# Performance work log

Measured on AMD Instinct MI355X. Metric: run time of the kernel, lower is better.

The kernel has to match this reference:

```python
import jax, jax.numpy as jnp
import numpy as np

EPS = 1e-5  # BatchNorm1d default eps


def xyz2sphere(xyz):
    # xyz: (..., 3) -> (rho, theta/pi, phi/(2pi)+0.5)
    rho = jnp.sqrt(jnp.sum(xyz * xyz, axis=-1, keepdims=True))
    safe_rho = jnp.where(rho == 0, 1.0, rho)
    theta = jnp.arccos(jnp.clip(xyz[..., 2:3] / safe_rho, -1.0, 1.0))
    theta = jnp.where(rho == 0, 0.0, theta) / jnp.pi
    phi = jnp.arctan2(xyz[..., 1:2], xyz[..., 0:1]) / (2.0 * jnp.pi) + 0.5
    return jnp.concatenate([rho, theta, phi], axis=-1)


def _conv_bn_relu(x, w, b, g, be):
    # x: (M, nsample, Cin); 1x1 Conv1d == per-point linear over channel dim
    y = jnp.einsum('mnc,oc->mno', x, w) + b
    mean = jnp.mean(y, axis=(0, 1))
    var = jnp.var(y, axis=(0, 1))  # biased var, matches torch BN training mode
    return jax.nn.relu(g * (y - mean) * jax.lax.rsqrt(var + EPS) + be)


def setup_inputs() -> dict:
    N, NS, CF = 32768, 32, 64
    key = jax.random.key(0)
    ks = jax.random.split(key, 8)
    center = jax.random.normal(ks[0], (N, 3), dtype=jnp.float32)
    normal = jax.random.normal(ks[1], (N, 3), dtype=jnp.float32)
    feature = jax.random.normal(ks[2], (N, CF), dtype=jnp.float32)
    group_idx = jax.random.randint(ks[3], (N, NS), 0, N)
    offset = jnp.full((1,), N, dtype=jnp.int32)
    s = 0.05
    return {
        'center': center, 'normal': normal, 'feature': feature,
        'offset': offset, 'group_idx': group_idx,
        'w0': jax.random.normal(ks[4], (64, 73), dtype=jnp.float32) * s,
        'b0': jnp.zeros((64,), jnp.float32), 'g0': jnp.ones((64,), jnp.float32), 'be0': jnp.zeros((64,), jnp.float32),
        'w1': jax.random.normal(ks[5], (64, 64), dtype=jnp.float32) * s,
        'b1': jnp.zeros((64,), jnp.float32), 'g1': jnp.ones((64,), jnp.float32), 'be1': jnp.zeros((64,), jnp.float32),
        'w2': jax.random.normal(ks[6], (128, 64), dtype=jnp.float32) * s,
        'b2': jnp.zeros((128,), jnp.float32), 'g2': jnp.ones((128,), jnp.float32), 'be2': jnp.zeros((128,), jnp.float32),
    }


def reference(center, normal, feature, offset, group_idx,
              w0, b0, g0, be0, w1, b1, g1, be1, w2, b2, g2, be2):
    # stride=1: new_center == center, M == N
    group_center = center[group_idx]            # (M, NS, 3)
    group_normal = normal[group_idx]            # (M, NS, 3)
    gcn = group_center - center[:, None, :]     # center-relative coords
    gcn = jnp.concatenate([gcn, xyz2sphere(gcn)], axis=-1)  # return_polar=True -> (M, NS, 6)
    x = jnp.concatenate([gcn, group_normal, feature[group_idx]], axis=-1)  # (M, NS, 73)
    x = _conv_bn_relu(x, w0, b0, g0, be0)
    x = _conv_bn_relu(x, w1, b1, g1, be1)
    x = _conv_bn_relu(x, w2, b2, g2, be2)
    new_feature = jnp.max(x, axis=1)            # max-pool over neighborhood -> (M, 128)
    return (center, normal, new_feature, offset)
```

## Files before the change

### kernel.cpp

```cpp
#include <hip/hip_runtime.h>
#include <hip/hip_bf16.h>
#include <math.h>


typedef __attribute__((ext_vector_type(8))) short short8;
typedef __attribute__((ext_vector_type(4))) float f32x4;

constexpr int NS = 32;
constexpr int GRIDS = 1280;
constexpr float BN_EPS = 1e-5f;
constexpr float INV_PI  = 0.31830988618379067f;
constexpr float INV_2PI = 0.15915494309189535f;

__device__ __forceinline__ short cvt_bf16(float f) {
    unsigned u = __float_as_uint(f);
    u = (u + 0x7FFFu + ((u >> 16) & 1u)) >> 16;
    return (short)u;
}

__global__ __launch_bounds__(256) void feat2bf(
    const float* __restrict__ feature, short* __restrict__ fb, int n8)
{
    int i = blockIdx.x * 256 + threadIdx.x;
    if (i >= n8) return;
    const float4* src = (const float4*)(feature + (size_t)i * 8);
    float4 a = src[0], b = src[1];
    short8 v;
    v[0]=cvt_bf16(a.x); v[1]=cvt_bf16(a.y); v[2]=cvt_bf16(a.z); v[3]=cvt_bf16(a.w);
    v[4]=cvt_bf16(b.x); v[5]=cvt_bf16(b.y); v[6]=cvt_bf16(b.z); v[7]=cvt_bf16(b.w);
    *(short8*)(fb + (size_t)i * 8) = v;
}

__global__ __launch_bounds__(256) void prep_cn(
    const float* __restrict__ center, const float* __restrict__ normal,
    float* __restrict__ cn, int N)
{
    int i = blockIdx.x * 256 + threadIdx.x;
    if (i >= N) return;
    float4 a, b;
    a.x = center[i*3+0]; a.y = center[i*3+1]; a.z = center[i*3+2];
    a.w = normal[i*3+0];
    b.x = normal[i*3+1]; b.y = normal[i*3+2]; b.z = 0.f; b.w = 0.f;
    *(float4*)(cn + (size_t)i * 8)     = a;
    *(float4*)(cn + (size_t)i * 8 + 4) = b;
}

__global__ __launch_bounds__(256) void prep_weights(
    const float* __restrict__ w0, const float* __restrict__ w1,
    const float* __restrict__ w2,
    short* __restrict__ wf0, short* __restrict__ wf1, short* __restrict__ wf2)
{
    int i = blockIdx.x * 256 + threadIdx.x;
    int l = i & 63;
    int f = i >> 6;
    float vals[8];
    short* dh;
    if (f < 12) {
        int kt = f >> 2, nt = f & 3;
        int n = nt * 16 + (l & 15);
        int k0 = kt * 32 + (l >> 4) * 8;
        for (int j = 0; j < 8; ++j) {
            int kn = k0 + j;
            float v;
            if (kn < 64)       v = w0[n * 73 + 9 + kn];
            else if (kn < 70)  v = w0[n * 73 + (kn - 64)];
            else if (kn == 70) v = w0[n * 73 + 6];
            else if (kn == 72) v = w0[n * 73 + 7];
            else if (kn == 73) v = w0[n * 73 + 8];
            else v = 0.f;
            vals[j] = v;
        }
        dh = wf0 + (size_t)f * 512 + l * 8;
    } else if (f < 20) {
        int ff = f - 12;
        int kt = ff >> 2, nt = ff & 3;
        int n = nt * 16 + (l & 15);
        int k0 = kt * 32 + (l >> 4) * 8;
        for (int j = 0; j < 8; ++j) vals[j] = w1[n * 64 + k0 + j];
        dh = wf1 + (size_t)ff * 512 + l * 8;
    } else if (f < 36) {
        int ff = f - 20;
        int kt = ff >> 3, nt = ff & 7;
        int n = nt * 16 + (l & 15);
        int k0 = kt * 32 + (l >> 4) * 8;
        for (int j = 0; j < 8; ++j) vals[j] = w2[n * 64 + k0 + j];
        dh = wf2 + (size_t)ff * 512 + l * 8;
    } else return;
    for (int j = 0; j < 8; ++j) dh[j] = cvt_bf16(vals[j]);
}

template <int STAGE>
__global__ __launch_bounds__(256, (STAGE == 2 ? 4 : 5)) void stage_kernel(
    const float* __restrict__ center, const float* __restrict__ normal,
    const float* __restrict__ feature, const short* __restrict__ fb,
    const float* __restrict__ cn, const int* __restrict__ gidx,
    const short* __restrict__ wf0, const short* __restrict__ wf1,
    const short* __restrict__ wf2,
    const float* __restrict__ b0, const float* __restrict__ b1,
    const float* __restrict__ b2,
    const float* __restrict__ g0, const float* __restrict__ be0,
    const float* __restrict__ g1, const float* __restrict__ be1,
    const float* __restrict__ fstats, float* __restrict__ part,
    float* __restrict__ ymax, float* __restrict__ ymin,
    int ntiles, float inv_cnt)
{
    __shared__ __align__(16) short Xs[64 * 128];
    __shared__ __align__(16) short X1s[(STAGE >= 1) ? 64 * 64 : 16];

    const int t    = threadIdx.x;
    const int lane = t & 63;
    const int wv   = __builtin_amdgcn_readfirstlane(t >> 6);
    const int ln   = lane & 15;
    const int kg   = lane >> 4;
    const int rs   = ln & 7;
    const int chW  = wv * 16 + ln;

    short8 W0[3];
#pragma unroll
    for (int kt = 0; kt < 3; ++kt)
        W0[kt] = *(const short8*)(wf0 + (size_t)((kt*4 + wv) * 64 + lane) * 8);
    short8 W1[2];
    if constexpr (STAGE >= 1) {
#pragma unroll
        for (int kt = 0; kt < 2; ++kt)
            W1[kt] = *(const short8*)(wf1 + (size_t)((kt*4 + wv) * 64 + lane) * 8);
    }
    short8 W2[2][2];
    if constexpr (STAGE == 2) {
#pragma unroll
        for (int nti = 0; nti < 2; ++nti)
#pragma unroll
            for (int kt = 0; kt < 2; ++kt) {
                int ff = kt * 8 + (wv * 2 + nti);
                W2[nti][kt] = *(const short8*)(wf2 + (size_t)(ff * 64 + lane) * 8);
            }
    }

    const float bb0 = b0[chW];
    float bb1 = 0.f, bb2a = 0.f, bb2b = 0.f;
    float a0v = 0.f, c0v = 0.f, a1v = 0.f, c1v = 0.f;
    if constexpr (STAGE >= 1) {
        bb1 = b1[chW];
        float mean = fstats[chW] * inv_cnt;
        float var  = fstats[64 + chW] * inv_cnt - mean * mean;
        a0v = g0[chW] * rsqrtf(fmaxf(var, 0.f) + BN_EPS);
        c0v = be0[chW] - a0v * mean;
    }
    if constexpr (STAGE == 2) {
        bb2a = b2[wv * 32 + ln];
        bb2b = b2[wv * 32 + 16 + ln];
        float mean = fstats[128 + chW] * inv_cnt;
        float var  = fstats[192 + chW] * inv_cnt - mean * mean;
        a1v = g1[chW] * rsqrtf(fmaxf(var, 0.f) + BN_EPS);
        c1v = be1[chW] - a1v * mean;
    }

    if (t < 128) {
        int r = t >> 1, u = 10 + (t & 1);
        short8 z; z[0]=0;z[1]=0;z[2]=0;z[3]=0;z[4]=0;z[5]=0;z[6]=0;z[7]=0;
        *(short8*)(Xs + r * 128 + ((u ^ (r & 7)) * 8)) = z;
    }

    constexpr int NT = (STAGE == 2) ? 2 : 1;
    float ssum[NT], ssq[NT];
#pragma unroll
    for (int nt = 0; nt < NT; ++nt) { ssum[nt] = 0.f; ssq[nt] = 0.f; }

    for (int tile = blockIdx.x; tile < ntiles; tile += gridDim.x) {
        const int m0 = tile * 2;
        __syncthreads();
        {
            const int s = t & 63, h = wv;
            const int m = m0 + (s >> 5);
            const int j = gidx[m * NS + (s & 31)];
            short* xr = Xs + s * 128;
            const int rx = s & 7;
            if (fb) {
                const uint4* fp = (const uint4*)(fb + (size_t)j * 64);
                uint4 v0 = fp[2 * h], v1 = fp[2 * h + 1];
                *(uint4*)(xr + (((2 * h)     ^ rx) * 8)) = v0;
                *(uint4*)(xr + (((2 * h + 1) ^ rx) * 8)) = v1;
            } else {
                const float4* fp = (const float4*)(feature + (size_t)j * 64 + h * 16);
#pragma unroll
                for (int q = 0; q < 2; ++q) {
                    float4 a = fp[2 * q], b = fp[2 * q + 1];
                    short8 v;
                    v[0]=cvt_bf16(a.x); v[1]=cvt_bf16(a.y); v[2]=cvt_bf16(a.z); v[3]=cvt_bf16(a.w);
                    v[4]=cvt_bf16(b.x); v[5]=cvt_bf16(b.y); v[6]=cvt_bf16(b.z); v[7]=cvt_bf16(b.w);
                    *(short8*)(xr + (((2 * h + q) ^ rx) * 8)) = v;
                }
            }
            if (h == 0) {
                float cjx, cjy, cjz, nx, cmx, cmy, cmz;
                if (cn) {
                    float4 cj = *(const float4*)(cn + (size_t)j * 8);
                    float4 cm = *(const float4*)(cn + (size_t)m * 8);
                    cjx=cj.x; cjy=cj.y; cjz=cj.z; nx=cj.w;
                    cmx=cm.x; cmy=cm.y; cmz=cm.z;
                } else {
                    cjx=center[j*3+0]; cjy=center[j*3+1]; cjz=center[j*3+2];
                    nx=normal[j*3+0];
                    cmx=center[m*3+0]; cmy=center[m*3+1]; cmz=center[m*3+2];
                }
                float gx = cjx - cmx, gy = cjy - cmy, gz = cjz - cmz;
                float rho = sqrtf(gx*gx + gy*gy + gz*gz);
                float th = 0.f;
                if (rho > 0.f) th = acosf(fminf(1.f, fmaxf(-1.f, gz / rho))) * INV_PI;
                float ph = atan2f(gy, gx) * INV_2PI + 0.5f;
                short8 v;
                v[0]=cvt_bf16(gx);  v[1]=cvt_bf16(gy); v[2]=cvt_bf16(gz);
                v[3]=cvt_bf16(rho); v[4]=cvt_bf16(th); v[5]=cvt_bf16(ph);
                v[6]=cvt_bf16(nx);  v[7]=0;
                *(short8*)(xr + ((8 ^ rx) * 8)) = v;
            } else if (h == 1) {
                float ny, nz;
                if (cn) {
                    float4 w = *(const float4*)(cn + (size_t)j * 8 + 4);
                    ny = w.x; nz = w.y;
                } else {
                    ny = normal[j*3+1]; nz = normal[j*3+2];
                }
                short8 v; v[0]=cvt_bf16(ny); v[1]=cvt_bf16(nz);
                v[2]=0;v[3]=0;v[4]=0;v[5]=0;v[6]=0;v[7]=0;
                *(short8*)(xr + ((9 ^ rx) * 8)) = v;
            }
        }
        __syncthreads();
#pragma unroll 2
        for (int mt = 0; mt < 4; ++mt) {
            const short* arow = Xs + (mt * 16 + ln) * 128;
            f32x4 acc = {bb0, bb0, bb0, bb0};
#pragma unroll
            for (int kt = 0; kt < 3; ++kt) {
                short8 A = *(const short8*)(arow + (((kt*4 + kg) ^ rs) * 8));
                acc = __builtin_amdgcn_mfma_f32_16x16x32_bf16(A, W0[kt], acc, 0, 0, 0);
            }
            if constexpr (STAGE == 0) {
#pragma unroll
                for (int r = 0; r < 4; ++r) {
                    float y = acc[r];
                    ssum[0] += y; ssq[0] += y * y;
                }
            } else {
#pragma unroll
                for (int r = 0; r < 4; ++r) {
                    int row = mt * 16 + kg * 4 + r;
                    float x1 = fmaxf(a0v * acc[r] + c0v, 0.f);
                    X1s[row * 64 + ((((chW >> 3) ^ (row & 7)) << 3) | (chW & 7))] = cvt_bf16(x1);
                }
            }
        }
        if constexpr (STAGE >= 1) {
            __syncthreads();
#pragma unroll 2
            for (int mt = 0; mt < 4; ++mt) {
                const short* arow = X1s + (mt * 16 + ln) * 64;
                f32x4 acc = {bb1, bb1, bb1, bb1};
#pragma unroll
                for (int kt = 0; kt < 2; ++kt) {
                    short8 A = *(const short8*)(arow + (((kt*4 + kg) ^ rs) * 8));
                    acc = __builtin_amdgcn_mfma_f32_16x16x32_bf16(A, W1[kt], acc, 0, 0, 0);
                }
                if constexpr (STAGE == 1) {
#pragma unroll
                    for (int r = 0; r < 4; ++r) {
                        float y = acc[r];
                        ssum[0] += y; ssq[0] += y * y;
                    }
                } else {
#pragma unroll
                    for (int r = 0; r < 4; ++r) {
                        int row = mt * 16 + kg * 4 + r;
                        float x2 = fmaxf(a1v * acc[r] + c1v, 0.f);
                        Xs[row * 128 + ((((chW >> 3) ^ (row & 7)) << 3) | (chW & 7))] = cvt_bf16(x2);
                    }
                }
            }
        }
        if constexpr (STAGE == 2) {
            __syncthreads();
#pragma unroll
            for (int p = 0; p < 2; ++p) {
                float mx0 = -3.402823466e38f, mn0 = 3.402823466e38f;
                float mx1 = -3.402823466e38f, mn1 = 3.402823466e38f;
#pragma unroll
                for (int mh = 0; mh < 2; ++mh) {
                    const int mt = p * 2 + mh;
                    const short* arow = Xs + (mt * 16 + ln) * 128;
                    short8 A0 = *(const short8*)(arow + (((kg)     ^ rs) * 8));
                    short8 A1 = *(const short8*)(arow + (((4 + kg) ^ rs) * 8));
                    f32x4 acc = {bb2a, bb2a, bb2a, bb2a};
                    acc = __builtin_amdgcn_mfma_f32_16x16x32_bf16(A0, W2[0][0], acc, 0, 0, 0);
                    acc = __builtin_amdgcn_mfma_f32_16x16x32_bf16(A1, W2[0][1], acc, 0, 0, 0);
#pragma unroll
                    for (int r = 0; r < 4; ++r) {
                        float y = acc[r];
                        ssum[0] += y; ssq[0] += y * y;
                        mx0 = fmaxf(mx0, y); mn0 = fminf(mn0, y);
                    }
                    f32x4 acd = {bb2b, bb2b, bb2b, bb2b};
                    acd = __builtin_amdgcn_mfma_f32_16x16x32_bf16(A0, W2[1][0], acd, 0, 0, 0);
                    acd = __builtin_amdgcn_mfma_f32_16x16x32_bf16(A1, W2[1][1], acd, 0, 0, 0);
#pragma unroll
                    for (int r = 0; r < 4; ++r) {
                        float y = acd[r];
                        ssum[1] += y; ssq[1] += y * y;
                        mx1 = fmaxf(mx1, y); mn1 = fminf(mn1, y);
                    }
                }
                mx0 = fmaxf(mx0, __shfl_xor(mx0, 16)); mn0 = fminf(mn0, __shfl_xor(mn0, 16));
                mx0 = fmaxf(mx0, __shfl_xor(mx0, 32)); mn0 = fminf(mn0, __shfl_xor(mn0, 32));
                mx1 = fmaxf(mx1, __shfl_xor(mx1, 16)); mn1 = fminf(mn1, __shfl_xor(mn1, 16));
                mx1 = fmaxf(mx1, __shfl_xor(mx1, 32)); mn1 = fminf(mn1, __shfl_xor(mn1, 32));
                if (lane < 16) {
                    size_t base = (size_t)(m0 + p) * 128 + wv * 32 + ln;
                    ymax[base]      = mx0; ymin[base]      = mn0;
                    ymax[base + 16] = mx1; ymin[base + 16] = mn1;
                }
            }
        }
    }

    float* pb = part + (size_t)blockIdx.x * 256;
#pragma unroll
    for (int nt = 0; nt < NT; ++nt) {
        float v = ssum[nt], q = ssq[nt];
        v += __shfl_xor(v, 16); q += __shfl_xor(q, 16);
        v += __shfl_xor(v, 32); q += __shfl_xor(q, 32);
        if (lane < 16) {
            constexpr int NCH = (STAGE == 2) ? 128 : 64;
            int c = (STAGE == 2) ? (wv * 32 + nt * 16 + ln) : (wv * 16 + ln);
            pb[c] = v; pb[NCH + c] = q;
        }
    }
}

__global__ __launch_bounds__(256) void reduce_partials(
    const float* __restrict__ part, float* __restrict__ fstats,
    int base, int nblocks)
{
    __shared__ float red[256];
    int c = blockIdx.x;
    float s = 0.f;
    for (int b = threadIdx.x; b < nblocks; b += 256)
        s += part[(size_t)b * 256 + c];
    red[threadIdx.x] = s;
    __syncthreads();
    for (int off = 128; off > 0; off >>= 1) {
        if (threadIdx.x < off) red[threadIdx.x] += red[threadIdx.x + off];
        __syncthreads();
    }
    if (threadIdx.x == 0) fstats[base + c] = red[0];
}

__global__ __launch_bounds__(256) void final_kernel(
    const float* __restrict__ center, const float* __restrict__ normal,
    const int* __restrict__ offs,
    const float* __restrict__ g2, const float* __restrict__ be2,
    const float* __restrict__ fstats,
    const float* __restrict__ ymax, const float* __restrict__ ymin,
    float* __restrict__ out, int N, float inv_cnt)
{
    int i = blockIdx.x * 256 + threadIdx.x;
    int nc = N * 3;
    int nf = N * 128;
    int total = 2 * nc + nf + 1;
    if (i >= total) return;
    if (i < nc) {
        out[i] = center[i];
    } else if (i < 2 * nc) {
        out[i] = normal[i - nc];
    } else if (i < 2 * nc + nf) {
        int idx = i - 2 * nc;
        int c = idx & 127;
        float mean = fstats[256 + c] * inv_cnt;
        float var  = fstats[384 + c] * inv_cnt - mean * mean;
        float a = g2[c] * rsqrtf(fmaxf(var, 0.f) + BN_EPS);
        float v = (a >= 0.f) ? ymax[idx] : ymin[idx];
        out[i] = fmaxf(a * (v - mean) + be2[c], 0.f);
    } else {
        out[i] = (float)offs[0];
    }
}

extern "C" void kernel_launch(void* const* d_in, const int* in_sizes, int n_in,
                              void* d_out, int out_size, void* d_ws, size_t ws_size,
                              hipStream_t stream)
{
    const float* center  = (const float*)d_in[0];
    const float* normal  = (const float*)d_in[1];
    const float* feature = (const float*)d_in[2];
    const int*   offs    = (const int*)d_in[3];
    const int*   gidx    = (const int*)d_in[4];
    const float* w0  = (const float*)d_in[5];
    const float* b0  = (const float*)d_in[6];
    const float* g0  = (const float*)d_in[7];
    const float* be0 = (const float*)d_in[8];
    const float* w1  = (const float*)d_in[9];
    const float* b1  = (const float*)d_in[10];
    const float* g1  = (const float*)d_in[11];
    const float* be1 = (const float*)d_in[12];
    const float* w2  = (const float*)d_in[13];
    const float* b2  = (const float*)d_in[14];
    const float* g2  = (const float*)d_in[15];
    const float* be2 = (const float*)d_in[16];

    const int N = in_sizes[0] / 3;
    const int ntiles = N / 2;
    const float inv_cnt = 1.0f / (float)((size_t)N * NS);

    float* out = (float*)d_out;
    float* out_nf = out + (size_t)2 * N * 3;

    float* wsf    = (float*)d_ws;
    float* fstats = wsf;
    float* part   = wsf + 512;
    float* ymin   = part + (size_t)GRIDS * 256;
    short* wbase  = (short*)(ymin + (size_t)N * 128);
    short* wf0 = wbase;
    short* wf1 = wf0 + 12 * 512;
    short* wf2 = wf1 + 8 * 512;
    short* wend = wf2 + 16 * 512;

    short* featbf = wend;
    float* cn     = (float*)(featbf + (size_t)N * 64);
    size_t need = (size_t)((char*)(cn + (size_t)N * 8) - (char*)d_ws);
    const bool has_tab = (ws_size >= need);
    const short* fbp = has_tab ? featbf : nullptr;
    const float* cnp = has_tab ? cn : nullptr;

    dim3 blk(256);

    prep_weights<<<dim3(9), blk, 0, stream>>>(w0, w1, w2, wf0, wf1, wf2);
    if (has_tab) {
        int n8 = N * 8;
        feat2bf<<<dim3((n8 + 255) / 256), blk, 0, stream>>>(feature, featbf, n8);
        prep_cn<<<dim3((N + 255) / 256), blk, 0, stream>>>(center, normal, cn, N);
    }

    stage_kernel<0><<<dim3(GRIDS), blk, 0, stream>>>(center, normal, feature,
        fbp, cnp, gidx, wf0, wf1, wf2, b0, b1, b2,
        g0, be0, g1, be1, fstats, part, out_nf, ymin, ntiles, inv_cnt);
    reduce_partials<<<dim3(128), blk, 0, stream>>>(part, fstats, 0, GRIDS);

    stage_kernel<1><<<dim3(GRIDS), blk, 0, stream>>>(center, normal, feature,
        fbp, cnp, gidx, wf0, wf1, wf2, b0, b1, b2,
        g0, be0, g1, be1, fstats, part, out_nf, ymin, ntiles, inv_cnt);
    reduce_partials<<<dim3(128), blk, 0, stream>>>(part, fstats, 128, GRIDS);

    stage_kernel<2><<<dim3(GRIDS), blk, 0, stream>>>(center, normal, feature,
        fbp, cnp, gidx, wf0, wf1, wf2, b0, b1, b2,
        g0, be0, g1, be1, fstats, part, out_nf, ymin, ntiles, inv_cnt);
    reduce_partials<<<dim3(256), blk, 0, stream>>>(part, fstats, 256, GRIDS);

    int total = 2 * N * 3 + N * 128 + 1;
    final_kernel<<<dim3((total + 255) / 256), blk, 0, stream>>>(
        center, normal, offs, g2, be2, fstats, out_nf, ymin, out, N, inv_cnt);
}
```

Before: 225.4 us.

## Load gathered features straight into MFMA operand registers, skip LDS staging

Gathered bf16 feature rows are now read directly from global memory into the MFMA A-operand registers instead of first being written to a 64x128 shared tile. Only the small geometry/normal part (16 channels) still goes through a compact padded shared buffer, and stage 2 gets its own X2s buffer for layer-2 activations. The intent is to drop LDS write/read traffic and shrink shared memory for better occupancy. The trade-off is more scattered global loads issued per lane, which may hurt coalescing. Stage 2 also moves to a smaller grid.

```diff
diff --git a/kernel.cpp b/kernel.cpp
--- a/kernel.cpp
+++ b/kernel.cpp
@@ -7,7 +7,8 @@
 typedef __attribute__((ext_vector_type(4))) float f32x4;
 
 constexpr int NS = 32;
-constexpr int GRIDS = 1280;
+constexpr int GRID01 = 1280;
+constexpr int GRID2  = 1024;
 constexpr float BN_EPS = 1e-5f;
 constexpr float INV_PI  = 0.31830988618379067f;
 constexpr float INV_2PI = 0.15915494309189535f;
@@ -104,8 +105,9 @@
     float* __restrict__ ymax, float* __restrict__ ymin,
     int ntiles, float inv_cnt)
 {
-    __shared__ __align__(16) short Xs[64 * 128];
+    __shared__ __align__(16) short Xg[64 * 20 + 16];
     __shared__ __align__(16) short X1s[(STAGE >= 1) ? 64 * 64 : 16];
+    __shared__ __align__(16) short X2s[(STAGE == 2) ? 64 * 64 : 16];
 
     const int t    = threadIdx.x;
     const int lane = t & 63;
@@ -155,11 +157,9 @@
         c1v = be1[chW] - a1v * mean;
     }
 
-    if (t < 128) {
-        int r = t >> 1, u = 10 + (t & 1);
-        short8 z; z[0]=0;z[1]=0;z[2]=0;z[3]=0;z[4]=0;z[5]=0;z[6]=0;z[7]=0;
-        *(short8*)(Xs + r * 128 + ((u ^ (r & 7)) * 8)) = z;
-    }
+    short8 zero8;
+    zero8[0]=0;zero8[1]=0;zero8[2]=0;zero8[3]=0;
+    zero8[4]=0;zero8[5]=0;zero8[6]=0;zero8[7]=0;
 
     constexpr int NT = (STAGE == 2) ? 2 : 1;
     float ssum[NT], ssq[NT];
@@ -169,29 +169,12 @@
     for (int tile = blockIdx.x; tile < ntiles; tile += gridDim.x) {
         const int m0 = tile * 2;
         __syncthreads();
+
         {
-            const int s = t & 63, h = wv;
-            const int m = m0 + (s >> 5);
-            const int j = gidx[m * NS + (s & 31)];
-            short* xr = Xs + s * 128;
-            const int rx = s & 7;
-            if (fb) {
-                const uint4* fp = (const uint4*)(fb + (size_t)j * 64);
-                uint4 v0 = fp[2 * h], v1 = fp[2 * h + 1];
-                *(uint4*)(xr + (((2 * h)     ^ rx) * 8)) = v0;
-                *(uint4*)(xr + (((2 * h + 1) ^ rx) * 8)) = v1;
-            } else {
-                const float4* fp = (const float4*)(feature + (size_t)j * 64 + h * 16);
-#pragma unroll
-                for (int q = 0; q < 2; ++q) {
-                    float4 a = fp[2 * q], b = fp[2 * q + 1];
-                    short8 v;
-                    v[0]=cvt_bf16(a.x); v[1]=cvt_bf16(a.y); v[2]=cvt_bf16(a.z); v[3]=cvt_bf16(a.w);
-                    v[4]=cvt_bf16(b.x); v[5]=cvt_bf16(b.y); v[6]=cvt_bf16(b.z); v[7]=cvt_bf16(b.w);
-                    *(short8*)(xr + (((2 * h + q) ^ rx) * 8)) = v;
-                }
-            }
-            if (h == 0) {
+            const int s = t & 63;
+            if (wv == 0) {
+                const int m = m0 + (s >> 5);
+                const int j = gidx[m * NS + (s & 31)];
                 float cjx, cjy, cjz, nx, cmx, cmy, cmz;
                 if (cn) {
                     float4 cj = *(const float4*)(cn + (size_t)j * 8);
@@ -212,8 +195,10 @@
                 v[0]=cvt_bf16(gx);  v[1]=cvt_bf16(gy); v[2]=cvt_bf16(gz);
                 v[3]=cvt_bf16(rho); v[4]=cvt_bf16(th); v[5]=cvt_bf16(ph);
                 v[6]=cvt_bf16(nx);  v[7]=0;
-                *(short8*)(xr + ((8 ^ rx) * 8)) = v;
-            } else if (h == 1) {
+                *(short8*)(Xg + s * 20 + (s >> 4) * 4) = v;
+            } else if (wv == 1) {
+                const int m = m0 + (s >> 5);
+                const int j = gidx[m * NS + (s & 31)];
                 float ny, nz;
                 if (cn) {
                     float4 w = *(const float4*)(cn + (size_t)j * 8 + 4);
@@ -223,19 +208,39 @@
                 }
                 short8 v; v[0]=cvt_bf16(ny); v[1]=cvt_bf16(nz);
                 v[2]=0;v[3]=0;v[4]=0;v[5]=0;v[6]=0;v[7]=0;
-                *(short8*)(xr + ((9 ^ rx) * 8)) = v;
-            }
-        }
+                *(short8*)(Xg + s * 20 + (s >> 4) * 4 + 8) = v;
+            }
+        }
+
+        int jv[4];
+#pragma unroll
+        for (int mt = 0; mt < 4; ++mt)
+            jv[mt] = gidx[m0 * 32 + mt * 16 + ln];
+
         __syncthreads();
-#pragma unroll 2
+
+#pragma unroll
         for (int mt = 0; mt < 4; ++mt) {
-            const short* arow = Xs + (mt * 16 + ln) * 128;
+            const int j = jv[mt];
+            short8 A0, A1;
+            if (fb) {
+                A0 = *(const short8*)(fb + (size_t)j * 64 + kg * 8);
+                A1 = *(const short8*)(fb + (size_t)j * 64 + 32 + kg * 8);
+            } else {
+                const float* fp = feature + (size_t)j * 64 + kg * 8;
+#pragma unroll
+                for (int q = 0; q < 8; ++q) {
+                    A0[q] = cvt_bf16(fp[q]);
+                    A1[q] = cvt_bf16(fp[32 + q]);
+                }
+            }
+            short8 A2 = zero8;
+            if (kg < 2)
+                A2 = *(const short8*)(Xg + (mt * 16 + ln) * 20 + mt * 4 + kg * 8);
             f32x4 acc = {bb0, bb0, bb0, bb0};
-#pragma unroll
-            for (int kt = 0; kt < 3; ++kt) {
-                short8 A = *(const short8*)(arow + (((kt*4 + kg) ^ rs) * 8));
-                acc = __builtin_amdgcn_mfma_f32_16x16x32_bf16(A, W0[kt], acc, 0, 0, 0);
-            }
+            acc = __builtin_amdgcn_mfma_f32_16x16x32_bf16(A0, W0[0], acc, 0, 0, 0);
+            acc = __builtin_amdgcn_mfma_f32_16x16x32_bf16(A1, W0[1], acc, 0, 0, 0);
+            acc = __builtin_amdgcn_mfma_f32_16x16x32_bf16(A2, W0[2], acc, 0, 0, 0);
             if constexpr (STAGE == 0) {
 #pragma unroll
                 for (int r = 0; r < 4; ++r) {
@@ -273,7 +278,7 @@
                     for (int r = 0; r < 4; ++r) {
                         int row = mt * 16 + kg * 4 + r;
                         float x2 = fmaxf(a1v * acc[r] + c1v, 0.f);
-                        Xs[row * 128 + ((((chW >> 3) ^ (row & 7)) << 3) | (chW & 7))] = cvt_bf16(x2);
+                        X2s[row * 64 + ((((chW >> 3) ^ (row & 7)) << 3) | (chW & 7))] = cvt_bf16(x2);
                     }
                 }
             }
@@ -287,7 +292,7 @@
 #pragma unroll
                 for (int mh = 0; mh < 2; ++mh) {
                     const int mt = p * 2 + mh;
-                    const short* arow = Xs + (mt * 16 + ln) * 128;
+                    const short* arow = X2s + (mt * 16 + ln) * 64;
                     short8 A0 = *(const short8*)(arow + (((kg)     ^ rs) * 8));
                     short8 A1 = *(const short8*)(arow + (((4 + kg) ^ rs) * 8));
                     f32x4 acc = {bb2a, bb2a, bb2a, bb2a};
@@ -416,7 +421,7 @@
     float* wsf    = (float*)d_ws;
     float* fstats = wsf;
     float* part   = wsf + 512;
-    float* ymin   = part + (size_t)GRIDS * 256;
+    float* ymin   = part + (size_t)GRID01 * 256;
     short* wbase  = (short*)(ymin + (size_t)N * 128);
     short* wf0 = wbase;
     short* wf1 = wf0 + 12 * 512;
@@ -439,20 +444,20 @@
         prep_cn<<<dim3((N + 255) / 256), blk, 0, stream>>>(center, normal, cn, N);
     }
 
-    stage_kernel<0><<<dim3(GRIDS), blk, 0, stream>>>(center, normal, feature,
+    stage_kernel<0><<<dim3(GRID01), blk, 0, stream>>>(center, normal, feature,
         fbp, cnp, gidx, wf0, wf1, wf2, b0, b1, b2,
         g0, be0, g1, be1, fstats, part, out_nf, ymin, ntiles, inv_cnt);
-    reduce_partials<<<dim3(128), blk, 0, stream>>>(part, fstats, 0, GRIDS);
-
-    stage_kernel<1><<<dim3(GRIDS), blk, 0, stream>>>(center, normal, feature,
+    reduce_partials<<<dim3(128), blk, 0, stream>>>(part, fstats, 0, GRID01);
+
+    stage_kernel<1><<<dim3(GRID01), blk, 0, stream>>>(center, normal, feature,
         fbp, cnp, gidx, wf0, wf1, wf2, b0, b1, b2,
         g0, be0, g1, be1, fstats, part, out_nf, ymin, ntiles, inv_cnt);
-    reduce_partials<<<dim3(128), blk, 0, stream>>>(part, fstats, 128, GRIDS);
-
-    stage_kernel<2><<<dim3(GRIDS), blk, 0, stream>>>(center, normal, feature,
+    reduce_partials<<<dim3(128), blk, 0, stream>>>(part, fstats, 128, GRID01);
+
+    stage_kernel<2><<<dim3(GRID2), blk, 0, stream>>>(center, normal, feature,
         fbp, cnp, gidx, wf0, wf1, wf2, b0, b1, b2,
         g0, be0, g1, be1, fstats, part, out_nf, ymin, ntiles, inv_cnt);
-    reduce_partials<<<dim3(256), blk, 0, stream>>>(part, fstats, 256, GRIDS);
+    reduce_partials<<<dim3(256), blk, 0, stream>>>(part, fstats, 256, GRID2);
 
     int total = 2 * N * 3 + N * 128 + 1;
     final_kernel<<<dim3((total + 255) / 256), blk, 0, stream>>>(
```

Result: slower. 331.1 us (+46.9%).
